# Optimization experiments

Measured on AMD Instinct MI355X. Metric: run time of the kernel, lower is better.

## Reference

```python
import jax, jax.numpy as jnp
import numpy as np

N_CODES = 1024
D = 128
BETA = 0.25


def setup_inputs() -> dict:
    key = jax.random.key(0)
    k1, k2 = jax.random.split(key)
    z = jax.random.normal(k1, (8, D, 4096), dtype=jnp.float32)  # (B, D, T)
    # nn.init.uniform_(codebook.weight, -1/n_codes, 1/n_codes)
    codebook = jax.random.uniform(
        k2, (N_CODES, D), dtype=jnp.float32,
        minval=-1.0 / N_CODES, maxval=1.0 / N_CODES)
    return {"z": z, "codebook": codebook}


def reference(z, codebook):
    B, D_, T = z.shape
    z_t = jnp.transpose(z, (0, 2, 1))           # (B, T, D)
    flat = z_t.reshape(B * T, D_)               # (BT, D)
    dist = (jnp.sum(flat * flat, axis=1, keepdims=True)
            - 2.0 * flat @ codebook.T
            + jnp.sum(codebook * codebook, axis=1)[None, :])
    codes = jnp.argmin(dist, axis=1)            # (BT,)
    z_q = codebook[codes].reshape(B, T, D_)     # (B, T, D)
    commit = jnp.mean((z_t - jax.lax.stop_gradient(z_q)) ** 2)
    codebk = jnp.mean((z_q - jax.lax.stop_gradient(z_t)) ** 2)
    loss = codebk + BETA * commit
    # straight-through estimator
    z_q_st = z_t + jax.lax.stop_gradient(z_q - z_t)
    z_q_out = jnp.transpose(z_q_st, (0, 2, 1))  # (B, D, T)
    return (z_q_out, codes.reshape(B, T), loss,
            dist.reshape(B, T, codebook.shape[0]))
```

## Files before the change

kernel.cpp:

```cpp
#include <hip/hip_runtime.h>

typedef __attribute__((ext_vector_type(8))) short short8;
typedef __attribute__((ext_vector_type(4))) float f32x4;

namespace {
constexpr long long OFF_CODES = 4194304;
constexpr long long OFF_LOSS  = 4227072;
constexpr long long OFF_DIST  = 4227073;
constexpr float EPS = 5e-4f;
constexpr size_t WS_LACC = 0;
constexpr size_t WS_SCF  = 1024;
constexpr size_t WS_SZF  = 8192;
constexpr size_t WS_FLAG = 139264;
constexpr size_t WS_CBH  = 270336;
}

__device__ __forceinline__ unsigned short bf_rne(float v) {
  unsigned int u = __float_as_uint(v);
  unsigned int r = u + 0x7FFFu + ((u >> 16) & 1u);
  return (unsigned short)(r >> 16);
}

__global__ __launch_bounds__(256) void vq_prep(
    const float* __restrict__ cb, unsigned short* __restrict__ cbh,
    float* __restrict__ scf, double* lacc)
{
  const int tid = threadIdx.x;
  const int row = blockIdx.x * 4 + (tid >> 6);
  const int d = tid & 63;
  float v0 = cb[row * 128 + d];
  float v1 = cb[row * 128 + 64 + d];
  cbh[row * 128 + d]      = bf_rne(v0);
  cbh[row * 128 + 64 + d] = bf_rne(v1);
  float q0 = v0 * v0, q1 = v1 * v1;
  double s = (double)q0 + (double)q1;
#pragma unroll
  for (int msk = 1; msk <= 32; msk <<= 1) s += __shfl_xor(s, msk);
  if (d == 0) scf[row] = (float)s;
  if (blockIdx.x == 0 && tid == 0) *lacc = 0.0;
}

template <int JT0>
__device__ __forceinline__ void half_pass(
    const unsigned short* __restrict__ pb, const short8 (&Ah)[2][4],
    const float (&szr)[2][4], const float* __restrict__ scfl,
    int w, int lj, int lg, int R0, float* __restrict__ out,
    float (&m1)[8], float (&m2)[8], int (&i1)[8])
{
  f32x4 acc[2][8];
#pragma unroll
  for (int u = 0; u < 8; ++u) {
    acc[0][u] = (f32x4){0.f, 0.f, 0.f, 0.f};
    acc[1][u] = (f32x4){0.f, 0.f, 0.f, 0.f};
#pragma unroll
    for (int ks = 0; ks < 4; ++ks) {
      short8 bh = *reinterpret_cast<const short8*>(pb + (size_t)(JT0 + u) * 2048 + ks * 32);
      acc[0][u] = __builtin_amdgcn_mfma_f32_16x16x32_bf16(Ah[0][ks], bh, acc[0][u], 0, 0, 0);
      acc[1][u] = __builtin_amdgcn_mfma_f32_16x16x32_bf16(Ah[1][ks], bh, acc[1][u], 0, 0, 0);
    }
  }
  float sc[8];
#pragma unroll
  for (int u = 0; u < 8; ++u) sc[u] = scfl[w * 256 + (JT0 + u) * 16 + lj];
#pragma unroll
  for (int tt = 0; tt < 2; ++tt)
#pragma unroll
    for (int r = 0; r < 4; ++r) {
      const int s = tt * 4 + r;
      const float sz = szr[tt][r];
      const int row = R0 + tt * 16 + lg * 4 + r;
      float* orow = out + OFF_DIST + (size_t)row * 1024 + w * 256 + JT0 * 16 + lj;
#pragma unroll
      for (int u = 0; u < 8; ++u) {
        float dv = (sz - 2.0f * acc[tt][u][r]) + sc[u];
        bool lt1 = dv < m1[s];
        float o1 = m1[s];
        m2[s] = lt1 ? o1 : fminf(m2[s], dv);
        m1[s] = lt1 ? dv : o1;
        i1[s] = lt1 ? (w * 256 + (JT0 + u) * 16 + lj) : i1[s];
        orow[u * 16] = dv;
      }
    }
}

__global__ __launch_bounds__(256, 2) void vq_main(
    const float* __restrict__ z, const unsigned short* __restrict__ cbh,
    const float* __restrict__ scf, float* __restrict__ szf,
    unsigned int* __restrict__ flags, float* __restrict__ out)
{
  __shared__ __align__(16) unsigned short zh[32 * 136];
  __shared__ double part[32][8];
  __shared__ float szl[32];
  __shared__ float scfl[1024];
  __shared__ float rm1[4][32], rm2[4][32];
  __shared__ int   ri1[4][32];

  const int tid = threadIdx.x;
  const int R0 = blockIdx.x * 32;
  const int b  = R0 >> 12;
  const int t0 = R0 & 4095;
  const float* zb = z + (size_t)b * 524288;

#pragma unroll
  for (int k = 0; k < 4; ++k) scfl[k * 256 + tid] = scf[k * 256 + tid];

  {
    double ps = 0.0;
    int t = tid & 31;
#pragma unroll
    for (int k = 0; k < 16; ++k) {
      int d = k * 8 + (tid >> 5);
      float v = zb[(size_t)d * 4096 + t0 + t];
      float q = v * v; ps += (double)q;
      zh[t * 136 + d] = bf_rne(v);
    }
    part[t][tid >> 5] = ps;
  }
  __syncthreads();
  if (tid < 32) {
    double s = 0.0;
#pragma unroll
    for (int g = 0; g < 8; ++g) s += part[tid][g];
    float sz = (float)s;
    szl[tid] = sz;
    szf[R0 + tid] = sz;
  }
  __syncthreads();

  const int w = tid >> 6, l = tid & 63, lj = l & 15, lg = l >> 4;

  short8 Ah[2][4];
#pragma unroll
  for (int tt = 0; tt < 2; ++tt)
#pragma unroll
    for (int ks = 0; ks < 4; ++ks)
      Ah[tt][ks] = *reinterpret_cast<const short8*>(
          &zh[(tt * 16 + lj) * 136 + ks * 32 + lg * 8]);
  float szr[2][4];
#pragma unroll
  for (int tt = 0; tt < 2; ++tt)
#pragma unroll
    for (int r = 0; r < 4; ++r) szr[tt][r] = szl[tt * 16 + lg * 4 + r];

  const unsigned short* pb = cbh + (size_t)(w * 256 + lj) * 128 + lg * 8;

  float m1[8], m2[8]; int i1[8];
#pragma unroll
  for (int s = 0; s < 8; ++s) { m1[s] = 3.4e38f; m2[s] = 3.4e38f; i1[s] = 0; }

  half_pass<0>(pb, Ah, szr, scfl, w, lj, lg, R0, out, m1, m2, i1);
  half_pass<8>(pb, Ah, szr, scfl, w, lj, lg, R0, out, m1, m2, i1);

#pragma unroll
  for (int s = 0; s < 8; ++s) {
    float a1 = m1[s]; int ai = i1[s]; float a2 = m2[s];
#pragma unroll
    for (int msk = 1; msk <= 8; msk <<= 1) {
      float b1 = __shfl_xor(a1, msk);
      int   bi = __shfl_xor(ai, msk);
      float b2 = __shfl_xor(a2, msk);
      bool keep = (a1 < b1) || (a1 == b1 && ai < bi);
      float lose = keep ? b1 : a1;
      a2 = fminf(fminf(a2, b2), lose);
      ai = keep ? ai : bi;
      a1 = keep ? a1 : b1;
    }
    if (lj == 0) {
      int t = (s >> 2) * 16 + lg * 4 + (s & 3);
      rm1[w][t] = a1; ri1[w][t] = ai; rm2[w][t] = a2;
    }
  }
  __syncthreads();
  if (tid < 32) {
    float f1 = rm1[0][tid]; int fi = ri1[0][tid]; float f2 = rm2[0][tid];
#pragma unroll
    for (int ww = 1; ww < 4; ++ww) {
      float b1 = rm1[ww][tid]; int bi = ri1[ww][tid]; float b2 = rm2[ww][tid];
      bool keep = (f1 < b1) || (f1 == b1 && fi < bi);
      float lose = keep ? b1 : f1;
      f2 = fminf(fminf(f2, b2), lose);
      fi = keep ? fi : bi;
      f1 = keep ? f1 : b1;
    }
    int R = R0 + tid;
    out[OFF_CODES + R] = (float)fi;
    flags[R] = (f2 - f1 <= EPS) ? 1u : 0u;
  }
}

__global__ __launch_bounds__(256) void vq_refine(
    const float* __restrict__ z, const float* __restrict__ cb,
    const float* __restrict__ scf, const float* __restrict__ szf,
    const unsigned int* __restrict__ flags, float* __restrict__ out)
{
  const int w = threadIdx.x >> 6, l = threadIdx.x & 63;
  const int R = blockIdx.x * 4 + w;
  if (!flags[R]) return;
  const int b = R >> 12, t = R & 4095;

  const float* drow = out + OFF_DIST + (size_t)R * 1024;
  float v[16];
#pragma unroll
  for (int k = 0; k < 16; ++k) v[k] = drow[k * 64 + l];
  float mn = 3.4e38f;
#pragma unroll
  for (int k = 0; k < 16; ++k) mn = fminf(mn, v[k]);
#pragma unroll
  for (int msk = 1; msk <= 32; msk <<= 1) mn = fminf(mn, __shfl_xor(mn, msk));
  const float thresh = mn + EPS;

  const double zd0 = (double)z[(size_t)b * 524288 + (size_t)l * 4096 + t];
  const double zd1 = (double)z[(size_t)b * 524288 + (size_t)(l + 64) * 4096 + t];
  const float szv = szf[R];

  float bestv = 3.4e38f; int bestj = 1 << 30;
#pragma unroll
  for (int k = 0; k < 16; ++k) {
    unsigned long long msk = __ballot(v[k] <= thresh);
    while (msk) {
      int s = __ffsll((unsigned long long)msk) - 1;
      msk &= msk - 1;
      int jc = k * 64 + s;
      float c0 = cb[(size_t)jc * 128 + l];
      float c1 = cb[(size_t)jc * 128 + 64 + l];
      double m = zd0 * (double)c0 + zd1 * (double)c1;
#pragma unroll
      for (int mm = 1; mm <= 32; mm <<= 1) m += __shfl_xor(m, mm);
      float m32 = (float)m;
      float dvex = (szv - 2.0f * m32) + scf[jc];
      if (dvex < bestv || (dvex == bestv && jc < bestj)) { bestv = dvex; bestj = jc; }
    }
  }
  if (l == 0) out[OFF_CODES + R] = (float)bestj;
}

__global__ __launch_bounds__(256) void vq_out_kernel(
    const float* __restrict__ z, const float* __restrict__ cb,
    float* __restrict__ out, double* __restrict__ lacc)
{
  __shared__ int ci[128];
  __shared__ float cq[128][129];
  __shared__ double lw[4];
  const int tid = threadIdx.x;
  const int b  = blockIdx.x >> 5;
  const int t0 = (blockIdx.x & 31) * 128;
  const int R0 = b * 4096 + t0;
  if (tid < 128) ci[tid] = (int)out[OFF_CODES + R0 + tid];
  __syncthreads();
  for (int r = 0; r < 128; r += 2) {
    int row = r + (tid >> 7);
    int d = tid & 127;
    cq[row][d] = cb[(size_t)ci[row] * 128 + d];
  }
  __syncthreads();
  double ls = 0.0;
  for (int dp = 0; dp < 128; dp += 2) {
    int d = dp + (tid >> 7);
    int t = tid & 127;
    size_t o = (size_t)b * 524288 + (size_t)d * 4096 + t0 + t;
    float zv = z[o];
    float q = cq[t][d];
    out[o] = zv + (q - zv);
    double dd = (double)q - (double)zv;
    ls += dd * dd;
  }
#pragma unroll
  for (int msk = 1; msk <= 32; msk <<= 1) ls += __shfl_xor(ls, msk);
  if ((tid & 63) == 0) lw[tid >> 6] = ls;
  __syncthreads();
  if (tid == 0) atomicAdd(lacc, lw[0] + lw[1] + lw[2] + lw[3]);
}

__global__ void vq_fin(const double* lacc, float* out) {
  if (threadIdx.x == 0 && blockIdx.x == 0)
    out[OFF_LOSS] = (float)(*lacc * (1.25 / 4194304.0));
}

extern "C" void kernel_launch(void* const* d_in, const int* in_sizes, int n_in,
                              void* d_out, int out_size, void* d_ws, size_t ws_size,
                              hipStream_t stream) {
  const float* z  = (const float*)d_in[0];
  const float* cb = (const float*)d_in[1];
  float* out = (float*)d_out;
  char* ws = (char*)d_ws;
  double* lacc = (double*)(ws + WS_LACC);
  float* scf = (float*)(ws + WS_SCF);
  float* szf = (float*)(ws + WS_SZF);
  unsigned int* flags = (unsigned int*)(ws + WS_FLAG);
  unsigned short* cbh = (unsigned short*)(ws + WS_CBH);

  vq_prep<<<256, 256, 0, stream>>>(cb, cbh, scf, lacc);
  vq_main<<<1024, 256, 0, stream>>>(z, cbh, scf, szf, flags, out);
  vq_refine<<<8192, 256, 0, stream>>>(z, cb, scf, szf, flags, out);
  vq_out_kernel<<<256, 256, 0, stream>>>(z, cb, out, lacc);
  vq_fin<<<1, 64, 0, stream>>>(lacc, out);
}
```

Before: 94.22 us.

## Split codebook across blocks and merge per-tile argmin partials in refine kernel

The main distance kernel now tiles over both rows and four 256-code slices, launching four times as many blocks. Each block writes partial min/second-min/index results to workspace, and the refine kernel merges these partials to produce the codes and decide whether a row needs exact refinement. The aim is more parallelism and higher occupancy (launch bounds raised to 3 blocks per SM, smaller accumulator set), with nontemporal stores for the large distance and output writes. In exchange, the z tile load and bf16 conversion are repeated per code slice, and the partial buffers add extra global traffic.

```diff
diff --git a/kernel.cpp b/kernel.cpp
--- a/kernel.cpp
+++ b/kernel.cpp
@@ -11,8 +11,10 @@
 constexpr size_t WS_LACC = 0;
 constexpr size_t WS_SCF  = 1024;
 constexpr size_t WS_SZF  = 8192;
-constexpr size_t WS_FLAG = 139264;
-constexpr size_t WS_CBH  = 270336;
+constexpr size_t WS_CBH  = 139264;
+constexpr size_t WS_PM1  = 401408;
+constexpr size_t WS_PM2  = 925696;
+constexpr size_t WS_PI1  = 1449984;
 }
 
 __device__ __forceinline__ unsigned short bf_rne(float v) {
@@ -40,69 +42,29 @@
   if (blockIdx.x == 0 && tid == 0) *lacc = 0.0;
 }
 
-template <int JT0>
-__device__ __forceinline__ void half_pass(
-    const unsigned short* __restrict__ pb, const short8 (&Ah)[2][4],
-    const float (&szr)[2][4], const float* __restrict__ scfl,
-    int w, int lj, int lg, int R0, float* __restrict__ out,
-    float (&m1)[8], float (&m2)[8], int (&i1)[8])
-{
-  f32x4 acc[2][8];
-#pragma unroll
-  for (int u = 0; u < 8; ++u) {
-    acc[0][u] = (f32x4){0.f, 0.f, 0.f, 0.f};
-    acc[1][u] = (f32x4){0.f, 0.f, 0.f, 0.f};
-#pragma unroll
-    for (int ks = 0; ks < 4; ++ks) {
-      short8 bh = *reinterpret_cast<const short8*>(pb + (size_t)(JT0 + u) * 2048 + ks * 32);
-      acc[0][u] = __builtin_amdgcn_mfma_f32_16x16x32_bf16(Ah[0][ks], bh, acc[0][u], 0, 0, 0);
-      acc[1][u] = __builtin_amdgcn_mfma_f32_16x16x32_bf16(Ah[1][ks], bh, acc[1][u], 0, 0, 0);
-    }
-  }
-  float sc[8];
-#pragma unroll
-  for (int u = 0; u < 8; ++u) sc[u] = scfl[w * 256 + (JT0 + u) * 16 + lj];
-#pragma unroll
-  for (int tt = 0; tt < 2; ++tt)
-#pragma unroll
-    for (int r = 0; r < 4; ++r) {
-      const int s = tt * 4 + r;
-      const float sz = szr[tt][r];
-      const int row = R0 + tt * 16 + lg * 4 + r;
-      float* orow = out + OFF_DIST + (size_t)row * 1024 + w * 256 + JT0 * 16 + lj;
-#pragma unroll
-      for (int u = 0; u < 8; ++u) {
-        float dv = (sz - 2.0f * acc[tt][u][r]) + sc[u];
-        bool lt1 = dv < m1[s];
-        float o1 = m1[s];
-        m2[s] = lt1 ? o1 : fminf(m2[s], dv);
-        m1[s] = lt1 ? dv : o1;
-        i1[s] = lt1 ? (w * 256 + (JT0 + u) * 16 + lj) : i1[s];
-        orow[u * 16] = dv;
-      }
-    }
-}
-
-__global__ __launch_bounds__(256, 2) void vq_main(
+__global__ __launch_bounds__(256, 3) void vq_main(
     const float* __restrict__ z, const unsigned short* __restrict__ cbh,
     const float* __restrict__ scf, float* __restrict__ szf,
-    unsigned int* __restrict__ flags, float* __restrict__ out)
+    float* __restrict__ pm1, float* __restrict__ pm2, int* __restrict__ pi1,
+    float* __restrict__ out)
 {
   __shared__ __align__(16) unsigned short zh[32 * 136];
   __shared__ double part[32][8];
   __shared__ float szl[32];
-  __shared__ float scfl[1024];
+  __shared__ float scfl[256];
   __shared__ float rm1[4][32], rm2[4][32];
   __shared__ int   ri1[4][32];
 
   const int tid = threadIdx.x;
-  const int R0 = blockIdx.x * 32;
+  const int jtile = blockIdx.x & 3;
+  const int rtile = blockIdx.x >> 2;
+  const int jb = jtile * 256;
+  const int R0 = rtile * 32;
   const int b  = R0 >> 12;
   const int t0 = R0 & 4095;
   const float* zb = z + (size_t)b * 524288;
 
-#pragma unroll
-  for (int k = 0; k < 4; ++k) scfl[k * 256 + tid] = scf[k * 256 + tid];
+  scfl[tid] = scf[jb + tid];
 
   {
     double ps = 0.0;
@@ -123,11 +85,12 @@
     for (int g = 0; g < 8; ++g) s += part[tid][g];
     float sz = (float)s;
     szl[tid] = sz;
-    szf[R0 + tid] = sz;
+    if (jtile == 0) szf[R0 + tid] = sz;
   }
   __syncthreads();
 
   const int w = tid >> 6, l = tid & 63, lj = l & 15, lg = l >> 4;
+  const int jw = jb + w * 64;
 
   short8 Ah[2][4];
 #pragma unroll
@@ -142,14 +105,50 @@
 #pragma unroll
     for (int r = 0; r < 4; ++r) szr[tt][r] = szl[tt * 16 + lg * 4 + r];
 
-  const unsigned short* pb = cbh + (size_t)(w * 256 + lj) * 128 + lg * 8;
+  const unsigned short* pb = cbh + (size_t)(jw + lj) * 128 + lg * 8;
+
+  f32x4 acc[2][4];
+#pragma unroll
+  for (int u = 0; u < 4; ++u) {
+    acc[0][u] = (f32x4){0.f, 0.f, 0.f, 0.f};
+    acc[1][u] = (f32x4){0.f, 0.f, 0.f, 0.f};
+    short8 bh0 = *reinterpret_cast<const short8*>(pb + (size_t)u * 2048);
+    short8 bh1 = *reinterpret_cast<const short8*>(pb + (size_t)u * 2048 + 32);
+    short8 bh2 = *reinterpret_cast<const short8*>(pb + (size_t)u * 2048 + 64);
+    short8 bh3 = *reinterpret_cast<const short8*>(pb + (size_t)u * 2048 + 96);
+    acc[0][u] = __builtin_amdgcn_mfma_f32_16x16x32_bf16(Ah[0][0], bh0, acc[0][u], 0, 0, 0);
+    acc[1][u] = __builtin_amdgcn_mfma_f32_16x16x32_bf16(Ah[1][0], bh0, acc[1][u], 0, 0, 0);
+    acc[0][u] = __builtin_amdgcn_mfma_f32_16x16x32_bf16(Ah[0][1], bh1, acc[0][u], 0, 0, 0);
+    acc[1][u] = __builtin_amdgcn_mfma_f32_16x16x32_bf16(Ah[1][1], bh1, acc[1][u], 0, 0, 0);
+    acc[0][u] = __builtin_amdgcn_mfma_f32_16x16x32_bf16(Ah[0][2], bh2, acc[0][u], 0, 0, 0);
+    acc[1][u] = __builtin_amdgcn_mfma_f32_16x16x32_bf16(Ah[1][2], bh2, acc[1][u], 0, 0, 0);
+    acc[0][u] = __builtin_amdgcn_mfma_f32_16x16x32_bf16(Ah[0][3], bh3, acc[0][u], 0, 0, 0);
+    acc[1][u] = __builtin_amdgcn_mfma_f32_16x16x32_bf16(Ah[1][3], bh3, acc[1][u], 0, 0, 0);
+  }
 
   float m1[8], m2[8]; int i1[8];
 #pragma unroll
   for (int s = 0; s < 8; ++s) { m1[s] = 3.4e38f; m2[s] = 3.4e38f; i1[s] = 0; }
 
-  half_pass<0>(pb, Ah, szr, scfl, w, lj, lg, R0, out, m1, m2, i1);
-  half_pass<8>(pb, Ah, szr, scfl, w, lj, lg, R0, out, m1, m2, i1);
+#pragma unroll
+  for (int tt = 0; tt < 2; ++tt)
+#pragma unroll
+    for (int r = 0; r < 4; ++r) {
+      const int s = tt * 4 + r;
+      const float sz = szr[tt][r];
+      float* orow = out + OFF_DIST
+                  + (size_t)(R0 + tt * 16 + lg * 4 + r) * 1024 + jw + lj;
+#pragma unroll
+      for (int u = 0; u < 4; ++u) {
+        float dv = (sz - 2.0f * acc[tt][u][r]) + scfl[w * 64 + u * 16 + lj];
+        bool lt1 = dv < m1[s];
+        float o1 = m1[s];
+        m2[s] = lt1 ? o1 : fminf(m2[s], dv);
+        m1[s] = lt1 ? dv : o1;
+        i1[s] = lt1 ? (jw + u * 16 + lj) : i1[s];
+        __builtin_nontemporal_store(dv, orow + u * 16);
+      }
+    }
 
 #pragma unroll
   for (int s = 0; s < 8; ++s) {
@@ -183,21 +182,37 @@
       f1 = keep ? f1 : b1;
     }
     int R = R0 + tid;
-    out[OFF_CODES + R] = (float)fi;
-    flags[R] = (f2 - f1 <= EPS) ? 1u : 0u;
+    pm1[jtile * 32768 + R] = f1;
+    pm2[jtile * 32768 + R] = f2;
+    pi1[jtile * 32768 + R] = fi;
   }
 }
 
 __global__ __launch_bounds__(256) void vq_refine(
     const float* __restrict__ z, const float* __restrict__ cb,
     const float* __restrict__ scf, const float* __restrict__ szf,
-    const unsigned int* __restrict__ flags, float* __restrict__ out)
+    const float* __restrict__ pm1, const float* __restrict__ pm2,
+    const int* __restrict__ pi1, float* __restrict__ out)
 {
   const int w = threadIdx.x >> 6, l = threadIdx.x & 63;
   const int R = blockIdx.x * 4 + w;
-  if (!flags[R]) return;
+
+  float f1 = pm1[R]; int fi = pi1[R]; float f2 = pm2[R];
+#pragma unroll
+  for (int jt = 1; jt < 4; ++jt) {
+    float b1 = pm1[jt * 32768 + R];
+    int   bi = pi1[jt * 32768 + R];
+    float b2 = pm2[jt * 32768 + R];
+    bool keep = (f1 < b1) || (f1 == b1 && fi < bi);
+    float lose = keep ? b1 : f1;
+    f2 = fminf(fminf(f2, b2), lose);
+    fi = keep ? fi : bi;
+    f1 = keep ? f1 : b1;
+  }
+  if (l == 0) out[OFF_CODES + R] = (float)fi;
+  if (f2 - f1 > EPS) return;
+
   const int b = R >> 12, t = R & 4095;
-
   const float* drow = out + OFF_DIST + (size_t)R * 1024;
   float v[16];
 #pragma unroll
@@ -260,7 +275,7 @@
     size_t o = (size_t)b * 524288 + (size_t)d * 4096 + t0 + t;
     float zv = z[o];
     float q = cq[t][d];
-    out[o] = zv + (q - zv);
+    __builtin_nontemporal_store(zv + (q - zv), out + o);
     double dd = (double)q - (double)zv;
     ls += dd * dd;
   }
@@ -286,12 +301,14 @@
   double* lacc = (double*)(ws + WS_LACC);
   float* scf = (float*)(ws + WS_SCF);
   float* szf = (float*)(ws + WS_SZF);
-  unsigned int* flags = (unsigned int*)(ws + WS_FLAG);
   unsigned short* cbh = (unsigned short*)(ws + WS_CBH);
+  float* pm1 = (float*)(ws + WS_PM1);
+  float* pm2 = (float*)(ws + WS_PM2);
+  int*   pi1 = (int*)(ws + WS_PI1);
 
   vq_prep<<<256, 256, 0, stream>>>(cb, cbh, scf, lacc);
-  vq_main<<<1024, 256, 0, stream>>>(z, cbh, scf, szf, flags, out);
-  vq_refine<<<8192, 256, 0, stream>>>(z, cb, scf, szf, flags, out);
+  vq_main<<<4096, 256, 0, stream>>>(z, cbh, scf, szf, pm1, pm2, pi1, out);
+  vq_refine<<<8192, 256, 0, stream>>>(z, cb, scf, szf, pm1, pm2, pi1, out);
   vq_out_kernel<<<256, 256, 0, stream>>>(z, cb, out, lacc);
   vq_fin<<<1, 64, 0, stream>>>(lacc, out);
 }
```

Result: slower. 135.3 us (+43.6%).

## Pre-swizzle codebook into MFMA fragment layout and split z-norm into separate kernel

Applied to the files above, without the earlier changes.

The codebook is rewritten in bf16 in the exact per-lane MFMA B-fragment order, so each wave's B loads become fully contiguous 16-byte accesses. The z squared-norm reduction moves out of vq_main into a new vq_szf kernel, which frees shared memory and registers; launch bounds rise to 4 blocks per CU. The main loop is rolled into four chunks of four tiles to cut register pressure. The cost is an extra kernel launch and a second full read of z.

```diff
diff --git a/kernel.cpp b/kernel.cpp
--- a/kernel.cpp
+++ b/kernel.cpp
@@ -12,7 +12,7 @@
 constexpr size_t WS_SCF  = 1024;
 constexpr size_t WS_SZF  = 8192;
 constexpr size_t WS_FLAG = 139264;
-constexpr size_t WS_CBH  = 270336;
+constexpr size_t WS_CBF  = 270336;
 }
 
 __device__ __forceinline__ unsigned short bf_rne(float v) {
@@ -21,109 +21,83 @@
   return (unsigned short)(r >> 16);
 }
 
-__global__ __launch_bounds__(256) void vq_prep(
-    const float* __restrict__ cb, unsigned short* __restrict__ cbh,
+__global__ __launch_bounds__(256) void vq_cbfrag(
+    const float* __restrict__ cb, unsigned short* __restrict__ cbf,
     float* __restrict__ scf, double* lacc)
 {
+  __shared__ double pn[4][16];
+  const int g = blockIdx.x;
   const int tid = threadIdx.x;
-  const int row = blockIdx.x * 4 + (tid >> 6);
-  const int d = tid & 63;
-  float v0 = cb[row * 128 + d];
-  float v1 = cb[row * 128 + 64 + d];
-  cbh[row * 128 + d]      = bf_rne(v0);
-  cbh[row * 128 + 64 + d] = bf_rne(v1);
-  float q0 = v0 * v0, q1 = v1 * v1;
-  double s = (double)q0 + (double)q1;
-#pragma unroll
-  for (int msk = 1; msk <= 32; msk <<= 1) s += __shfl_xor(s, msk);
-  if (d == 0) scf[row] = (float)s;
+  const int ks = tid >> 6, l = tid & 63, lg = l >> 4, lj = l & 15;
+  const float* src = cb + (size_t)(g * 16 + lj) * 128 + ks * 32 + lg * 8;
+  double s = 0.0;
+  short8 h;
+#pragma unroll
+  for (int e = 0; e < 8; ++e) {
+    float v = src[e];
+    float q = v * v;
+    s += (double)q;
+    h[e] = (short)bf_rne(v);
+  }
+  *reinterpret_cast<short8*>(cbf + (size_t)g * 2048 + (size_t)tid * 8) = h;
+  s += __shfl_xor(s, 16);
+  s += __shfl_xor(s, 32);
+  if (lg == 0) pn[ks][lj] = s;
+  __syncthreads();
+  if (tid < 16)
+    scf[g * 16 + tid] = (float)(pn[0][tid] + pn[1][tid] + pn[2][tid] + pn[3][tid]);
   if (blockIdx.x == 0 && tid == 0) *lacc = 0.0;
 }
 
-template <int JT0>
-__device__ __forceinline__ void half_pass(
-    const unsigned short* __restrict__ pb, const short8 (&Ah)[2][4],
-    const float (&szr)[2][4], const float* __restrict__ scfl,
-    int w, int lj, int lg, int R0, float* __restrict__ out,
-    float (&m1)[8], float (&m2)[8], int (&i1)[8])
-{
-  f32x4 acc[2][8];
-#pragma unroll
-  for (int u = 0; u < 8; ++u) {
-    acc[0][u] = (f32x4){0.f, 0.f, 0.f, 0.f};
-    acc[1][u] = (f32x4){0.f, 0.f, 0.f, 0.f};
-#pragma unroll
-    for (int ks = 0; ks < 4; ++ks) {
-      short8 bh = *reinterpret_cast<const short8*>(pb + (size_t)(JT0 + u) * 2048 + ks * 32);
-      acc[0][u] = __builtin_amdgcn_mfma_f32_16x16x32_bf16(Ah[0][ks], bh, acc[0][u], 0, 0, 0);
-      acc[1][u] = __builtin_amdgcn_mfma_f32_16x16x32_bf16(Ah[1][ks], bh, acc[1][u], 0, 0, 0);
-    }
-  }
-  float sc[8];
-#pragma unroll
-  for (int u = 0; u < 8; ++u) sc[u] = scfl[w * 256 + (JT0 + u) * 16 + lj];
-#pragma unroll
-  for (int tt = 0; tt < 2; ++tt)
-#pragma unroll
-    for (int r = 0; r < 4; ++r) {
-      const int s = tt * 4 + r;
-      const float sz = szr[tt][r];
-      const int row = R0 + tt * 16 + lg * 4 + r;
-      float* orow = out + OFF_DIST + (size_t)row * 1024 + w * 256 + JT0 * 16 + lj;
-#pragma unroll
-      for (int u = 0; u < 8; ++u) {
-        float dv = (sz - 2.0f * acc[tt][u][r]) + sc[u];
-        bool lt1 = dv < m1[s];
-        float o1 = m1[s];
-        m2[s] = lt1 ? o1 : fminf(m2[s], dv);
-        m1[s] = lt1 ? dv : o1;
-        i1[s] = lt1 ? (w * 256 + (JT0 + u) * 16 + lj) : i1[s];
-        orow[u * 16] = dv;
-      }
-    }
-}
-
-__global__ __launch_bounds__(256, 2) void vq_main(
-    const float* __restrict__ z, const unsigned short* __restrict__ cbh,
-    const float* __restrict__ scf, float* __restrict__ szf,
+__global__ __launch_bounds__(256) void vq_szf(
+    const float* __restrict__ z, float* __restrict__ szf)
+{
+  __shared__ double pn[64][4];
+  const int tid = threadIdx.x;
+  const int R0 = blockIdx.x * 64;
+  const int b = R0 >> 12, t0 = R0 & 4095;
+  const int t = tid & 63, dg = tid >> 6;
+  const float* zp = z + (size_t)b * 524288 + (size_t)dg * 32 * 4096 + t0 + t;
+  double s = 0.0;
+#pragma unroll
+  for (int d = 0; d < 32; ++d) {
+    float v = zp[(size_t)d * 4096];
+    float q = v * v;
+    s += (double)q;
+  }
+  pn[t][dg] = s;
+  __syncthreads();
+  if (tid < 64)
+    szf[R0 + tid] = (float)(pn[tid][0] + pn[tid][1] + pn[tid][2] + pn[tid][3]);
+}
+
+__global__ __launch_bounds__(256, 4) void vq_main(
+    const float* __restrict__ z, const unsigned short* __restrict__ cbf,
+    const float* __restrict__ scf, const float* __restrict__ szf,
     unsigned int* __restrict__ flags, float* __restrict__ out)
 {
   __shared__ __align__(16) unsigned short zh[32 * 136];
-  __shared__ double part[32][8];
+  __shared__ float scfl[1024];
   __shared__ float szl[32];
-  __shared__ float scfl[1024];
   __shared__ float rm1[4][32], rm2[4][32];
   __shared__ int   ri1[4][32];
 
   const int tid = threadIdx.x;
   const int R0 = blockIdx.x * 32;
-  const int b  = R0 >> 12;
-  const int t0 = R0 & 4095;
+  const int b = R0 >> 12, t0 = R0 & 4095;
   const float* zb = z + (size_t)b * 524288;
 
 #pragma unroll
   for (int k = 0; k < 4; ++k) scfl[k * 256 + tid] = scf[k * 256 + tid];
+  if (tid < 32) szl[tid] = szf[R0 + tid];
 
   {
-    double ps = 0.0;
     int t = tid & 31;
 #pragma unroll
     for (int k = 0; k < 16; ++k) {
       int d = k * 8 + (tid >> 5);
-      float v = zb[(size_t)d * 4096 + t0 + t];
-      float q = v * v; ps += (double)q;
-      zh[t * 136 + d] = bf_rne(v);
-    }
-    part[t][tid >> 5] = ps;
-  }
-  __syncthreads();
-  if (tid < 32) {
-    double s = 0.0;
-#pragma unroll
-    for (int g = 0; g < 8; ++g) s += part[tid][g];
-    float sz = (float)s;
-    szl[tid] = sz;
-    szf[R0 + tid] = sz;
+      zh[t * 136 + d] = bf_rne(zb[(size_t)d * 4096 + t0 + t]);
+    }
   }
   __syncthreads();
 
@@ -142,14 +116,46 @@
 #pragma unroll
     for (int r = 0; r < 4; ++r) szr[tt][r] = szl[tt * 16 + lg * 4 + r];
 
-  const unsigned short* pb = cbh + (size_t)(w * 256 + lj) * 128 + lg * 8;
-
   float m1[8], m2[8]; int i1[8];
 #pragma unroll
   for (int s = 0; s < 8; ++s) { m1[s] = 3.4e38f; m2[s] = 3.4e38f; i1[s] = 0; }
 
-  half_pass<0>(pb, Ah, szr, scfl, w, lj, lg, R0, out, m1, m2, i1);
-  half_pass<8>(pb, Ah, szr, scfl, w, lj, lg, R0, out, m1, m2, i1);
+  const unsigned short* pwave = cbf + (size_t)w * 16 * 2048 + (size_t)l * 8;
+
+#pragma unroll 1
+  for (int q = 0; q < 4; ++q) {
+    f32x4 acc[2][4];
+#pragma unroll
+    for (int u = 0; u < 4; ++u) {
+      acc[0][u] = (f32x4){0.f, 0.f, 0.f, 0.f};
+      acc[1][u] = (f32x4){0.f, 0.f, 0.f, 0.f};
+      const unsigned short* pg = pwave + (size_t)(q * 4 + u) * 2048;
+#pragma unroll
+      for (int ks = 0; ks < 4; ++ks) {
+        short8 bh = *reinterpret_cast<const short8*>(pg + ks * 512);
+        acc[0][u] = __builtin_amdgcn_mfma_f32_16x16x32_bf16(Ah[0][ks], bh, acc[0][u], 0, 0, 0);
+        acc[1][u] = __builtin_amdgcn_mfma_f32_16x16x32_bf16(Ah[1][ks], bh, acc[1][u], 0, 0, 0);
+      }
+    }
+#pragma unroll
+    for (int u = 0; u < 4; ++u) {
+      const int jj = w * 256 + (q * 4 + u) * 16 + lj;
+      const float sc = scfl[jj];
+#pragma unroll
+      for (int tt = 0; tt < 2; ++tt)
+#pragma unroll
+        for (int r = 0; r < 4; ++r) {
+          float dv = (szr[tt][r] - 2.0f * acc[tt][u][r]) + sc;
+          const int s = tt * 4 + r;
+          bool lt1 = dv < m1[s];
+          float o1 = m1[s];
+          m2[s] = lt1 ? o1 : fminf(m2[s], dv);
+          m1[s] = lt1 ? dv : o1;
+          i1[s] = lt1 ? jj : i1[s];
+          out[OFF_DIST + (size_t)(R0 + tt * 16 + lg * 4 + r) * 1024 + jj] = dv;
+        }
+    }
+  }
 
 #pragma unroll
   for (int s = 0; s < 8; ++s) {
@@ -287,10 +293,11 @@
   float* scf = (float*)(ws + WS_SCF);
   float* szf = (float*)(ws + WS_SZF);
   unsigned int* flags = (unsigned int*)(ws + WS_FLAG);
-  unsigned short* cbh = (unsigned short*)(ws + WS_CBH);
-
-  vq_prep<<<256, 256, 0, stream>>>(cb, cbh, scf, lacc);
-  vq_main<<<1024, 256, 0, stream>>>(z, cbh, scf, szf, flags, out);
+  unsigned short* cbf = (unsigned short*)(ws + WS_CBF);
+
+  vq_cbfrag<<<64, 256, 0, stream>>>(cb, cbf, scf, lacc);
+  vq_szf<<<512, 256, 0, stream>>>(z, szf);
+  vq_main<<<1024, 256, 0, stream>>>(z, cbf, scf, szf, flags, out);
   vq_refine<<<8192, 256, 0, stream>>>(z, cb, scf, szf, flags, out);
   vq_out_kernel<<<256, 256, 0, stream>>>(z, cb, out, lacc);
   vq_fin<<<1, 64, 0, stream>>>(lacc, out);
```

Result: faster. 79.23 us (median of 2 runs) (-15.9%).
